# Kernel tuning notes

Hardware: AMD Instinct MI355X
Metric: run time of the kernel (lower is better)

## Reference

```python
import jax, jax.numpy as jnp
import numpy as np

B, C, H, W = 8, 512, 64, 64
CQ = C // 8  # query/key projection dim


def setup_inputs() -> dict:
    key = jax.random.key(0)
    ks = jax.random.split(key, 8)
    s = 0.02
    return {
        "x": jax.random.normal(ks[0], (B, C, H, W), dtype=jnp.float32),
        "Wq": jax.random.normal(ks[1], (CQ, C), dtype=jnp.float32) * s,
        "bq": jax.random.normal(ks[2], (CQ,), dtype=jnp.float32) * s,
        "Wk": jax.random.normal(ks[3], (CQ, C), dtype=jnp.float32) * s,
        "bk": jax.random.normal(ks[4], (CQ,), dtype=jnp.float32) * s,
        "Wv": jax.random.normal(ks[5], (C, C), dtype=jnp.float32) * s,
        "bv": jax.random.normal(ks[6], (C,), dtype=jnp.float32) * s,
        "gamma": jax.random.normal(ks[7], (1,), dtype=jnp.float32) * 0.1,
    }


def reference(x, Wq, bq, Wk, bk, Wv, bv, gamma):
    b, c, h, w = x.shape
    n = h * w
    xf = x.reshape(b, c, n)                                  # [B,C,N]
    # 1x1 convs == per-pixel linear maps over channels
    q = jnp.einsum('dc,bcn->bdn', Wq, xf) + bq[:, None]       # [B,CQ,N]
    k = jnp.einsum('dc,bcn->bdn', Wk, xf) + bk[:, None]       # [B,CQ,N]
    v = jnp.einsum('dc,bcn->bdn', Wv, xf) + bv[:, None]       # [B,C,N]
    # attention[b, i, j] = softmax_j( q_i . k_j )
    attn = jax.nn.softmax(jnp.einsum('bdn,bdm->bnm', q, k), axis=-1)  # [B,N,N]
    # out[b, c, i] = sum_j v[b, c, j] * attn[b, i, j]
    out = jnp.einsum('bcj,bij->bci', v, attn).reshape(b, c, h, w)
    return gamma[0] * out + x
```

## Files before the change

kernel.cpp:

```cpp
#include <hip/hip_runtime.h>
#include <hip/hip_bf16.h>

#define BB 8
#define CC 512
#define NN 4096
#define CQ 64

typedef __bf16 bf16;
typedef __bf16 bf16x4 __attribute__((ext_vector_type(4)));
typedef __bf16 bf16x8 __attribute__((ext_vector_type(8)));
typedef float f32x4 __attribute__((ext_vector_type(4)));

__device__ __forceinline__ f32x4 mfma16(bf16x8 a, bf16x8 b, f32x4 c) {
    return __builtin_amdgcn_mfma_f32_16x16x32_bf16(a, b, c, 0, 0, 0);
}

#define BAR_LDS()                                            \
    do {                                                     \
        asm volatile("s_waitcnt lgkmcnt(0)" ::: "memory");   \
        __builtin_amdgcn_s_barrier();                        \
    } while (0)


__global__ __launch_bounds__(256) void k_transpose(const float* __restrict__ x,
                                                   bf16* __restrict__ xTt) {
    __shared__ float tile[64][65];
    const int b  = blockIdx.z;
    const int c0 = blockIdx.y * 64;
    const int n0 = blockIdx.x * 64;
    const int t  = threadIdx.x;

    const float* xp = x + ((size_t)b * CC + c0) * NN + n0;
#pragma unroll
    for (int r = 0; r < 16; ++r) {
        int c = r * 4 + (t >> 6);
        int n = t & 63;
        tile[c][n] = xp[(size_t)c * NN + n];
    }
    __syncthreads();
#pragma unroll
    for (int r = 0; r < 16; ++r) {
        int nl = r * 4 + (t >> 6);
        int cl = t & 63;
        size_t off = ((size_t)(b * 256 + (n0 >> 4) + (nl >> 4)) * 16 + (c0 >> 5) + (cl >> 5)) * 512
                   + (nl & 15) * 32 + (cl & 31);
        xTt[off] = (bf16)tile[cl][nl];
    }
}

__global__ __launch_bounds__(256) void k_castw(const float* __restrict__ Wq,
                                               const float* __restrict__ Wk,
                                               const float* __restrict__ Wv,
                                               bf16* __restrict__ Wqt,
                                               bf16* __restrict__ Wkt,
                                               bf16* __restrict__ Wvt) {
    int i = blockIdx.x * 256 + threadIdx.x;
    const int nqk = CQ * CC;
    const float* src;
    bf16* dst;
    int j;
    if (i < nqk) {
        src = Wq; dst = Wqt; j = i;
    } else if (i < 2 * nqk) {
        src = Wk; dst = Wkt; j = i - nqk;
    } else if (i < 2 * nqk + CC * CC) {
        src = Wv; dst = Wvt; j = i - 2 * nqk;
    } else {
        return;
    }
    int d = j >> 9;
    int c = j & 511;
    size_t off = ((size_t)(d >> 4) * 16 + (c >> 5)) * 512 + (d & 15) * 32 + (c & 31);
    dst[off] = (bf16)src[j];
}

__global__ __launch_bounds__(256) void k_proj_qk(const bf16* __restrict__ xTt,
                                                 const bf16* __restrict__ Wqt,
                                                 const bf16* __restrict__ Wkt,
                                                 const float* __restrict__ bq,
                                                 const float* __restrict__ bk,
                                                 bf16* __restrict__ qTt,
                                                 bf16* __restrict__ kTt) {
    const int b  = blockIdx.y;
    const int nt = blockIdx.x * 4 + (threadIdx.x >> 6);
    const int l  = threadIdx.x & 63;
    const int l15 = l & 15, lq = l >> 4;
    const int loff = l15 * 32 + lq * 8;

    f32x4 acc[8];
#pragma unroll
    for (int dt = 0; dt < 4; ++dt) {
        float bvq = bq[dt * 16 + l15];
        float bvk = bk[dt * 16 + l15];
        acc[dt]     = (f32x4){bvq, bvq, bvq, bvq};
        acc[4 + dt] = (f32x4){bvk, bvk, bvk, bvk};
    }

    const bf16* ap = xTt + ((size_t)(b * 256 + nt) * 16) * 512 + loff;
#pragma unroll 2
    for (int ct = 0; ct < 16; ++ct) {
        bf16x8 a = *(const bf16x8*)(ap + (size_t)ct * 512);
#pragma unroll
        for (int dt = 0; dt < 4; ++dt) {
            bf16x8 fq = *(const bf16x8*)(Wqt + ((size_t)dt * 16 + ct) * 512 + loff);
            acc[dt] = mfma16(a, fq, acc[dt]);
        }
#pragma unroll
        for (int dt = 0; dt < 4; ++dt) {
            bf16x8 fk = *(const bf16x8*)(Wkt + ((size_t)dt * 16 + ct) * 512 + loff);
            acc[4 + dt] = mfma16(a, fk, acc[4 + dt]);
        }
    }
#pragma unroll
    for (int dt = 0; dt < 4; ++dt) {
#pragma unroll
        for (int r = 0; r < 4; ++r) {
            size_t off = ((size_t)(b * 256 + nt) * 2 + (dt >> 1)) * 512
                       + (lq * 4 + r) * 32 + (dt & 1) * 16 + l15;
            qTt[off] = (bf16)acc[dt][r];
            kTt[off] = (bf16)acc[4 + dt][r];
        }
    }
}

__global__ __launch_bounds__(256, 2) void k_proj_v(const bf16* __restrict__ xTt,
                                                   const bf16* __restrict__ Wvt,
                                                   const float* __restrict__ bv,
                                                   bf16* __restrict__ vt) {
    const int b  = blockIdx.y;
    const int bx = blockIdx.x;
    const int w  = threadIdx.x >> 6;
    const int l  = threadIdx.x & 63;
    const int l15 = l & 15, lq = l >> 4;
    const int loff = l15 * 32 + lq * 8;

    f32x4 acc[8][4];
#pragma unroll
    for (int dt = 0; dt < 8; ++dt) {
        f32x4 binit;
#pragma unroll
        for (int r = 0; r < 4; ++r) binit[r] = bv[(w * 8 + dt) * 16 + lq * 4 + r];
#pragma unroll
        for (int nt = 0; nt < 4; ++nt) acc[dt][nt] = binit;
    }

    const bf16* ap = Wvt + ((size_t)(w * 8) * 16) * 512 + loff;
    const bf16* bp = xTt + ((size_t)(b * 256 + bx * 4) * 16) * 512 + loff;
#pragma unroll 1
    for (int ct = 0; ct < 16; ++ct) {
        bf16x8 bxf[4];
#pragma unroll
        for (int nt = 0; nt < 4; ++nt)
            bxf[nt] = *(const bf16x8*)(bp + ((size_t)nt * 16 + ct) * 512);
#pragma unroll
        for (int dt = 0; dt < 8; ++dt) {
            bf16x8 aW = *(const bf16x8*)(ap + ((size_t)dt * 16 + ct) * 512);
#pragma unroll
            for (int nt = 0; nt < 4; ++nt)
                acc[dt][nt] = mfma16(aW, bxf[nt], acc[dt][nt]);
        }
    }
#pragma unroll
    for (int dt = 0; dt < 8; ++dt) {
#pragma unroll
        for (int nt = 0; nt < 4; ++nt) {
#pragma unroll
            for (int r = 0; r < 4; ++r) {
                size_t off = ((size_t)(b * 32 + w * 8 + dt) * 128 + bx * 2 + (nt >> 1)) * 512
                           + (lq * 4 + r) * 32 + (nt & 1) * 16 + l15;
                vt[off] = (bf16)acc[dt][nt][r];
            }
        }
    }
}

__global__ __launch_bounds__(256, 2) void k_attn(const bf16* __restrict__ qTt,
                                                 const bf16* __restrict__ kTt,
                                                 const bf16* __restrict__ vt,
                                                 const float* __restrict__ x,
                                                 const float* __restrict__ gamma,
                                                 float* __restrict__ out) {
    __shared__ bf16  Pl[2][8][512];
    __shared__ bf16  Kl[2][4][512];
    __shared__ float Ll[8][16];

    const int b  = blockIdx.x & 7;
    const int ch = (blockIdx.x >> 3) & 1;
    const int i0 = (blockIdx.x >> 4) * 128;
    const int t  = threadIdx.x;
    const int w  = t >> 6;
    const int l  = t & 63;
    const int l15 = l & 15, lq = l >> 4;
    const int loff = l15 * 32 + lq * 8;

    const f32x4 zero4 = {0.f, 0.f, 0.f, 0.f};

    const bf16* kb = kTt + (size_t)b * 256 * 2 * 512;
    const bf16* qb = qTt + (size_t)b * 256 * 2 * 512;
    const bf16* vb = vt + ((size_t)b * 32 + ch * 16 + w * 4) * 128 * 512 + loff;

    bf16x8 qa[2][2];
#pragma unroll
    for (int e = 0; e < 2; ++e) {
        const bf16* qp = qb + ((size_t)((i0 >> 4) + w + e * 4) * 2) * 512 + loff;
        qa[e][0] = *(const bf16x8*)qp;
        qa[e][1] = *(const bf16x8*)(qp + 512);
    }

    f32x4 acc[4][8];
#pragma unroll
    for (int ct = 0; ct < 4; ++ct)
#pragma unroll
        for (int it = 0; it < 8; ++it) acc[ct][it] = zero4;
    float lsA = 0.f, lsB = 0.f;

    bf16x8 kcur;
    {
        bf16x8 k0 = *(const bf16x8*)(kb + (size_t)w * 512 + loff);
        *(bf16x8*)&Kl[0][w][l * 8] = k0;
        kcur = *(const bf16x8*)(kb + (size_t)(4 + w) * 512 + loff);
    }
    BAR_LDS();

#pragma unroll 2
    for (int jb = 0; jb < NN / 32; ++jb) {
        const int buf = jb & 1;

        bf16x8 knxt;
        {
            const int jk = (jb + 2) & (NN / 32 - 1);
            knxt = *(const bf16x8*)(kb + ((size_t)jk * 4 + w) * 512 + loff);
        }

        bf16x8 va[4];
#pragma unroll
        for (int ct = 0; ct < 4; ++ct)
            va[ct] = *(const bf16x8*)(vb + ((size_t)ct * 128 + jb) * 512);

        bf16x8 ka[4];
#pragma unroll
        for (int q = 0; q < 4; ++q)
            ka[q] = *(const bf16x8*)&Kl[buf][q][l * 8];

        f32x4 st[2][2];
#pragma unroll
        for (int e = 0; e < 2; ++e)
#pragma unroll
            for (int jt = 0; jt < 2; ++jt) {
                f32x4 s = mfma16(ka[jt * 2], qa[e][0], zero4);
                st[e][jt] = mfma16(ka[jt * 2 + 1], qa[e][1], s);
            }

        *(bf16x8*)&Kl[buf ^ 1][w][l * 8] = kcur;
        kcur = knxt;

#pragma unroll
        for (int e = 0; e < 2; ++e) {
            float rs = 0.f;
#pragma unroll
            for (int jt = 0; jt < 2; ++jt) {
                float p0 = __expf(st[e][jt][0]);
                float p1 = __expf(st[e][jt][1]);
                float p2 = __expf(st[e][jt][2]);
                float p3 = __expf(st[e][jt][3]);
                rs += (p0 + p1) + (p2 + p3);
                bf16x4 pk = {(bf16)p0, (bf16)p1, (bf16)p2, (bf16)p3};
                int g = jt * 2 + (lq >> 1);
                *(bf16x4*)&Pl[buf][w + e * 4][g * 128 + l15 * 8 + (lq & 1) * 4] = pk;
            }
            if (e == 0) lsA += rs; else lsB += rs;
        }

        BAR_LDS();

        __builtin_amdgcn_s_setprio(1);
        bf16x8 pc = *(const bf16x8*)&Pl[buf][0][l * 8];
        bf16x8 pn = *(const bf16x8*)&Pl[buf][1][l * 8];
#pragma unroll
        for (int it = 0; it < 8; ++it) {
            bf16x8 p2;
            if (it < 6) p2 = *(const bf16x8*)&Pl[buf][it + 2][l * 8];
            acc[0][it] = mfma16(va[0], pc, acc[0][it]);
            acc[1][it] = mfma16(va[1], pc, acc[1][it]);
            acc[2][it] = mfma16(va[2], pc, acc[2][it]);
            acc[3][it] = mfma16(va[3], pc, acc[3][it]);
            pc = pn;
            pn = p2;
        }
        __builtin_amdgcn_s_setprio(0);
    }

    lsA += __shfl_xor(lsA, 16);
    lsA += __shfl_xor(lsA, 32);
    lsB += __shfl_xor(lsB, 16);
    lsB += __shfl_xor(lsB, 32);
    if (l < 16) {
        Ll[w][l]     = lsA;
        Ll[w + 4][l] = lsB;
    }
    __syncthreads();

    const float g = gamma[0];
    float linv[8];
#pragma unroll
    for (int it = 0; it < 8; ++it) linv[it] = 1.0f / Ll[it][l15];

#pragma unroll
    for (int ct = 0; ct < 4; ++ct) {
#pragma unroll
        for (int it = 0; it < 8; ++it) {
#pragma unroll
            for (int r = 0; r < 4; ++r) {
                int c = ch * 256 + (w * 4 + ct) * 16 + lq * 4 + r;
                size_t idx = ((size_t)b * CC + c) * NN + i0 + it * 16 + l15;
                out[idx] = g * (acc[ct][it][r] * linv[it]) + x[idx];
            }
        }
    }
}

extern "C" void kernel_launch(void* const* d_in, const int* in_sizes, int n_in,
                              void* d_out, int out_size, void* d_ws, size_t ws_size,
                              hipStream_t stream) {
    const float* x     = (const float*)d_in[0];
    const float* Wq    = (const float*)d_in[1];
    const float* bq    = (const float*)d_in[2];
    const float* Wk    = (const float*)d_in[3];
    const float* bk    = (const float*)d_in[4];
    const float* Wv    = (const float*)d_in[5];
    const float* bv    = (const float*)d_in[6];
    const float* gamma = (const float*)d_in[7];
    float* out = (float*)d_out;

    char* p = (char*)d_ws;
    bf16* xTt = (bf16*)p; p += (size_t)BB * NN * CC * sizeof(bf16);
    bf16* qTt = (bf16*)p; p += (size_t)BB * NN * CQ * sizeof(bf16);
    bf16* kTt = (bf16*)p; p += (size_t)BB * NN * CQ * sizeof(bf16);
    bf16* vt  = (bf16*)p; p += (size_t)BB * CC * NN * sizeof(bf16);
    bf16* Wqt = (bf16*)p; p += (size_t)CQ * CC * sizeof(bf16);
    bf16* Wkt = (bf16*)p; p += (size_t)CQ * CC * sizeof(bf16);
    bf16* Wvt = (bf16*)p; p += (size_t)CC * CC * sizeof(bf16);

    k_transpose<<<dim3(NN / 64, CC / 64, BB), 256, 0, stream>>>(x, xTt);
    k_castw<<<(2 * CQ * CC + CC * CC + 255) / 256, 256, 0, stream>>>(Wq, Wk, Wv, Wqt, Wkt, Wvt);
    k_proj_qk<<<dim3(NN / 64, BB), 256, 0, stream>>>(xTt, Wqt, Wkt, bq, bk, qTt, kTt);
    k_proj_v<<<dim3(NN / 64, BB), 256, 0, stream>>>(xTt, Wvt, bv, vt);
    k_attn<<<512, 256, 0, stream>>>(qTt, kTt, vt, x, gamma, out);
}
```

Measured before the change: 227.5 us.

## Use 512-thread attention blocks covering all channels and software-pipeline QK with PV

The attention kernel now launches 256 blocks of 512 threads, so each block covers all 512 channels for its 128 queries. Each wave computes scores for 16 queries rather than 32, which removes the duplicated QK^T and exp work that the two channel-half blocks used to repeat. The loop is software-pipelined: the scores for key block jb are computed while the PV MFMAs consume the probabilities of block jb-1, with a prologue and an epilogue added, so only one barrier sits on the critical path per iteration. In exchange, register pressure per wave is higher, the grid has half as many blocks, and only four of the eight waves stage K tiles.

```diff
diff --git a/kernel.cpp b/kernel.cpp
--- a/kernel.cpp
+++ b/kernel.cpp
@@ -174,7 +174,7 @@
     }
 }
 
-__global__ __launch_bounds__(256, 2) void k_attn(const bf16* __restrict__ qTt,
+__global__ __launch_bounds__(512, 2) void k_attn(const bf16* __restrict__ qTt,
                                                  const bf16* __restrict__ kTt,
                                                  const bf16* __restrict__ vt,
                                                  const float* __restrict__ x,
@@ -185,8 +185,7 @@
     __shared__ float Ll[8][16];
 
     const int b  = blockIdx.x & 7;
-    const int ch = (blockIdx.x >> 3) & 1;
-    const int i0 = (blockIdx.x >> 4) * 128;
+    const int i0 = (blockIdx.x >> 3) * 128;
     const int t  = threadIdx.x;
     const int w  = t >> 6;
     const int l  = t & 63;
@@ -197,14 +196,13 @@
 
     const bf16* kb = kTt + (size_t)b * 256 * 2 * 512;
     const bf16* qb = qTt + (size_t)b * 256 * 2 * 512;
-    const bf16* vb = vt + ((size_t)b * 32 + ch * 16 + w * 4) * 128 * 512 + loff;
-
-    bf16x8 qa[2][2];
-#pragma unroll
-    for (int e = 0; e < 2; ++e) {
-        const bf16* qp = qb + ((size_t)((i0 >> 4) + w + e * 4) * 2) * 512 + loff;
-        qa[e][0] = *(const bf16x8*)qp;
-        qa[e][1] = *(const bf16x8*)(qp + 512);
+    const bf16* vb = vt + ((size_t)b * 32 + w * 4) * 128 * 512 + loff;
+
+    bf16x8 qa0, qa1;
+    {
+        const bf16* qp = qb + ((size_t)((i0 >> 4) + w) * 2) * 512 + loff;
+        qa0 = *(const bf16x8*)qp;
+        qa1 = *(const bf16x8*)(qp + 512);
     }
 
     f32x4 acc[4][8];
@@ -212,74 +210,82 @@
     for (int ct = 0; ct < 4; ++ct)
 #pragma unroll
         for (int it = 0; it < 8; ++it) acc[ct][it] = zero4;
-    float lsA = 0.f, lsB = 0.f;
+    float lsum = 0.f;
 
     bf16x8 kcur;
+    if (w < 4) {
+        bf16x8 k0 = *(const bf16x8*)(kb + (size_t)w * 512 + loff);
+        bf16x8 k1 = *(const bf16x8*)(kb + (size_t)(4 + w) * 512 + loff);
+        *(bf16x8*)&Kl[0][w][l * 8] = k0;
+        *(bf16x8*)&Kl[1][w][l * 8] = k1;
+        kcur = *(const bf16x8*)(kb + (size_t)(8 + w) * 512 + loff);
+    }
+    BAR_LDS();
+
     {
-        bf16x8 k0 = *(const bf16x8*)(kb + (size_t)w * 512 + loff);
-        *(bf16x8*)&Kl[0][w][l * 8] = k0;
-        kcur = *(const bf16x8*)(kb + (size_t)(4 + w) * 512 + loff);
+        bf16x8 ka[4];
+#pragma unroll
+        for (int q = 0; q < 4; ++q)
+            ka[q] = *(const bf16x8*)&Kl[0][q][l * 8];
+        f32x4 st[2];
+#pragma unroll
+        for (int jt = 0; jt < 2; ++jt) {
+            f32x4 s = mfma16(ka[jt * 2], qa0, zero4);
+            st[jt] = mfma16(ka[jt * 2 + 1], qa1, s);
+        }
+#pragma unroll
+        for (int jt = 0; jt < 2; ++jt) {
+            float p0 = __expf(st[jt][0]);
+            float p1 = __expf(st[jt][1]);
+            float p2 = __expf(st[jt][2]);
+            float p3 = __expf(st[jt][3]);
+            lsum += (p0 + p1) + (p2 + p3);
+            bf16x4 pk = {(bf16)p0, (bf16)p1, (bf16)p2, (bf16)p3};
+            int g = jt * 2 + (lq >> 1);
+            *(bf16x4*)&Pl[0][w][g * 128 + l15 * 8 + (lq & 1) * 4] = pk;
+        }
     }
     BAR_LDS();
 
 #pragma unroll 2
-    for (int jb = 0; jb < NN / 32; ++jb) {
+    for (int jb = 1; jb < NN / 32; ++jb) {
         const int buf = jb & 1;
+
+        bf16x8 va[4];
+#pragma unroll
+        for (int ct = 0; ct < 4; ++ct)
+            va[ct] = *(const bf16x8*)(vb + ((size_t)ct * 128 + jb - 1) * 512);
 
         bf16x8 knxt;
         {
             const int jk = (jb + 2) & (NN / 32 - 1);
-            knxt = *(const bf16x8*)(kb + ((size_t)jk * 4 + w) * 512 + loff);
-        }
-
-        bf16x8 va[4];
-#pragma unroll
-        for (int ct = 0; ct < 4; ++ct)
-            va[ct] = *(const bf16x8*)(vb + ((size_t)ct * 128 + jb) * 512);
+            if (w < 4)
+                knxt = *(const bf16x8*)(kb + ((size_t)jk * 4 + w) * 512 + loff);
+        }
 
         bf16x8 ka[4];
 #pragma unroll
         for (int q = 0; q < 4; ++q)
             ka[q] = *(const bf16x8*)&Kl[buf][q][l * 8];
 
-        f32x4 st[2][2];
-#pragma unroll
-        for (int e = 0; e < 2; ++e)
-#pragma unroll
-            for (int jt = 0; jt < 2; ++jt) {
-                f32x4 s = mfma16(ka[jt * 2], qa[e][0], zero4);
-                st[e][jt] = mfma16(ka[jt * 2 + 1], qa[e][1], s);
-            }
-
-        *(bf16x8*)&Kl[buf ^ 1][w][l * 8] = kcur;
+        __builtin_amdgcn_s_setprio(1);
+        f32x4 st[2];
+#pragma unroll
+        for (int jt = 0; jt < 2; ++jt) {
+            f32x4 s = mfma16(ka[jt * 2], qa0, zero4);
+            st[jt] = mfma16(ka[jt * 2 + 1], qa1, s);
+        }
+
+        if (w < 4)
+            *(bf16x8*)&Kl[buf ^ 1][w][l * 8] = kcur;
         kcur = knxt;
 
-#pragma unroll
-        for (int e = 0; e < 2; ++e) {
-            float rs = 0.f;
-#pragma unroll
-            for (int jt = 0; jt < 2; ++jt) {
-                float p0 = __expf(st[e][jt][0]);
-                float p1 = __expf(st[e][jt][1]);
-                float p2 = __expf(st[e][jt][2]);
-                float p3 = __expf(st[e][jt][3]);
-                rs += (p0 + p1) + (p2 + p3);
-                bf16x4 pk = {(bf16)p0, (bf16)p1, (bf16)p2, (bf16)p3};
-                int g = jt * 2 + (lq >> 1);
-                *(bf16x4*)&Pl[buf][w + e * 4][g * 128 + l15 * 8 + (lq & 1) * 4] = pk;
-            }
-            if (e == 0) lsA += rs; else lsB += rs;
-        }
-
-        BAR_LDS();
-
-        __builtin_amdgcn_s_setprio(1);
-        bf16x8 pc = *(const bf16x8*)&Pl[buf][0][l * 8];
-        bf16x8 pn = *(const bf16x8*)&Pl[buf][1][l * 8];
+        bf16x8 pc = *(const bf16x8*)&Pl[buf ^ 1][0][l * 8];
+        bf16x8 pn = *(const bf16x8*)&Pl[buf ^ 1][1][l * 8];
 #pragma unroll
         for (int it = 0; it < 8; ++it) {
             bf16x8 p2;
-            if (it < 6) p2 = *(const bf16x8*)&Pl[buf][it + 2][l * 8];
+            if (it < 6) p2 = *(const bf16x8*)&Pl[buf ^ 1][it + 2][l * 8];
             acc[0][it] = mfma16(va[0], pc, acc[0][it]);
             acc[1][it] = mfma16(va[1], pc, acc[1][it]);
             acc[2][it] = mfma16(va[2], pc, acc[2][it]);
@@ -288,16 +294,45 @@
             pn = p2;
         }
         __builtin_amdgcn_s_setprio(0);
-    }
-
-    lsA += __shfl_xor(lsA, 16);
-    lsA += __shfl_xor(lsA, 32);
-    lsB += __shfl_xor(lsB, 16);
-    lsB += __shfl_xor(lsB, 32);
-    if (l < 16) {
-        Ll[w][l]     = lsA;
-        Ll[w + 4][l] = lsB;
-    }
+
+#pragma unroll
+        for (int jt = 0; jt < 2; ++jt) {
+            float p0 = __expf(st[jt][0]);
+            float p1 = __expf(st[jt][1]);
+            float p2 = __expf(st[jt][2]);
+            float p3 = __expf(st[jt][3]);
+            lsum += (p0 + p1) + (p2 + p3);
+            bf16x4 pk = {(bf16)p0, (bf16)p1, (bf16)p2, (bf16)p3};
+            int g = jt * 2 + (lq >> 1);
+            *(bf16x4*)&Pl[buf][w][g * 128 + l15 * 8 + (lq & 1) * 4] = pk;
+        }
+
+        BAR_LDS();
+    }
+
+    {
+        bf16x8 va[4];
+#pragma unroll
+        for (int ct = 0; ct < 4; ++ct)
+            va[ct] = *(const bf16x8*)(vb + ((size_t)ct * 128 + 127) * 512);
+        bf16x8 pc = *(const bf16x8*)&Pl[1][0][l * 8];
+        bf16x8 pn = *(const bf16x8*)&Pl[1][1][l * 8];
+#pragma unroll
+        for (int it = 0; it < 8; ++it) {
+            bf16x8 p2;
+            if (it < 6) p2 = *(const bf16x8*)&Pl[1][it + 2][l * 8];
+            acc[0][it] = mfma16(va[0], pc, acc[0][it]);
+            acc[1][it] = mfma16(va[1], pc, acc[1][it]);
+            acc[2][it] = mfma16(va[2], pc, acc[2][it]);
+            acc[3][it] = mfma16(va[3], pc, acc[3][it]);
+            pc = pn;
+            pn = p2;
+        }
+    }
+
+    lsum += __shfl_xor(lsum, 16);
+    lsum += __shfl_xor(lsum, 32);
+    if (l < 16) Ll[w][l] = lsum;
     __syncthreads();
 
     const float g = gamma[0];
@@ -311,7 +346,7 @@
         for (int it = 0; it < 8; ++it) {
 #pragma unroll
             for (int r = 0; r < 4; ++r) {
-                int c = ch * 256 + (w * 4 + ct) * 16 + lq * 4 + r;
+                int c = (w * 4 + ct) * 16 + lq * 4 + r;
                 size_t idx = ((size_t)b * CC + c) * NN + i0 + it * 16 + l15;
                 out[idx] = g * (acc[ct][it][r] * linv[it]) + x[idx];
             }
@@ -345,5 +380,5 @@
     k_castw<<<(2 * CQ * CC + CC * CC + 255) / 256, 256, 0, stream>>>(Wq, Wk, Wv, Wqt, Wkt, Wvt);
     k_proj_qk<<<dim3(NN / 64, BB), 256, 0, stream>>>(xTt, Wqt, Wkt, bq, bk, qTt, kTt);
     k_proj_v<<<dim3(NN / 64, BB), 256, 0, stream>>>(xTt, Wvt, bv, vt);
-    k_attn<<<512, 256, 0, stream>>>(qTt, kTt, vt, x, gamma, out);
-}
+    k_attn<<<256, 512, 0, stream>>>(qTt, kTt, vt, x, gamma, out);
+}
```

Measured after the change: 254.2 us. 1.12x slower.
